# Performance work log

Hardware: AMD Instinct MI355X
Metric: run time of the kernel (lower is better)

Reference implementation:

```python
import jax, jax.numpy as jnp
import numpy as np

N_NODES = 100000
N_EDGES = 3200000
C_IN = 128
C_OUT = 128
K = 4

def setup_inputs() -> dict:
    key = jax.random.key(0)
    k1, k2, k3, k4, k5 = jax.random.split(key, 5)
    x = jax.random.normal(k1, (N_NODES, C_IN), dtype=jnp.float32)
    # per-edge Laplacian values, scaled so the Chebyshev recurrence stays bounded
    lap = jax.random.normal(k2, (N_EDGES,), dtype=jnp.float32) * 0.05
    stdv = 1.0 / np.sqrt(C_IN * K)
    weight = jax.random.uniform(k3, (K, C_IN, C_OUT), dtype=jnp.float32, minval=-stdv, maxval=stdv)
    bias = jax.random.uniform(k4, (C_OUT,), dtype=jnp.float32, minval=-stdv, maxval=stdv)
    edge_index = jax.random.randint(k5, (2, N_EDGES), 0, N_NODES, dtype=jnp.int64)
    return {"x": x, "lap": lap, "weight": weight, "bias": bias,
            "edge_index": edge_index, "num_nodes": N_NODES}

def _spmm(edge_index, lap, num_nodes, x):
    # y[row] += lap_e * x[col] for each edge e = (row, col)
    row, col = edge_index[0], edge_index[1]
    msgs = lap[:, None] * x[col]            # [E, C]
    return jax.ops.segment_sum(msgs, row, num_segments=num_nodes)

def reference(x, lap, weight, bias, edge_index, num_nodes):
    K_ = weight.shape[0]
    Tx_0 = x                                 # T_0(L) x = x
    out = Tx_0 @ weight[0]
    if K_ > 1:
        Tx_1 = _spmm(edge_index, lap, num_nodes, x)   # T_1(L) x = L x
        out = out + Tx_1 @ weight[1]
    for k in range(2, K_):
        Tx_2 = 2.0 * _spmm(edge_index, lap, num_nodes, Tx_1) - Tx_0
        out = out + Tx_2 @ weight[k]
        Tx_0, Tx_1 = Tx_1, Tx_2
    return out + bias
```

## Files before the change

### kernel.cpp

```cpp
#include <hip/hip_runtime.h>

#define N_NODES 100000
#define N_EDGES 3200000
#define ROWS_PAD 100032
#define N_BUCKETS 782
#define BUCKET_SHIFT 7

typedef __attribute__((ext_vector_type(8))) short bf16x8;
typedef __attribute__((ext_vector_type(4))) float f32x4;
typedef __attribute__((ext_vector_type(2))) float f32x2;

__device__ __forceinline__ unsigned short f2bf(float f) {
    unsigned u = __float_as_uint(f);
    unsigned r = (u + 0x7fffu + ((u >> 16) & 1u)) >> 16;
    return (unsigned short)r;
}
__device__ __forceinline__ float bflo(unsigned u) { return __uint_as_float(u << 16); }
__device__ __forceinline__ float bfhi(unsigned u) { return __uint_as_float(u & 0xffff0000u); }

__global__ void __launch_bounds__(256) k_convert_x(const float* __restrict__ x,
                                                   unsigned* __restrict__ xf8) {
    const int QTOT = ROWS_PAD * 32;
    for (int q = blockIdx.x * 256 + threadIdx.x; q < QTOT; q += 1024 * 256) {
        int r = q >> 5;
        f32x4 f = {0.f, 0.f, 0.f, 0.f};
        if (r < N_NODES) f = *(const f32x4*)(x + 4 * (size_t)q);
        int pk = __builtin_amdgcn_cvt_pk_fp8_f32(f.x, f.y, 0, false);
        pk = __builtin_amdgcn_cvt_pk_fp8_f32(f.z, f.w, pk, true);
        xf8[q] = (unsigned)pk;
    }
}

__global__ void k_convert_w(const float* __restrict__ w, unsigned short* __restrict__ wt) {
    int i = blockIdx.x * 256 + threadIdx.x;
    int m = i >> 14, rem = i & 16383, k = rem >> 7, c = rem & 127;
    wt[(m << 14) + (c << 7) + k] = f2bf(w[i]);
}

__global__ void __launch_bounds__(256) k_bhist(const int* __restrict__ ei, int* __restrict__ bcnt) {
    __shared__ int h[N_BUCKETS];
    for (int i = threadIdx.x; i < N_BUCKETS; i += 256) h[i] = 0;
    __syncthreads();
    int base = blockIdx.x * 8192;
#pragma unroll
    for (int i = 0; i < 32; ++i) {
        int e = base + threadIdx.x + i * 256;
        if (e < N_EDGES) atomicAdd(&h[ei[e] >> BUCKET_SHIFT], 1);
    }
    __syncthreads();
    for (int i = threadIdx.x; i < N_BUCKETS; i += 256)
        if (h[i]) atomicAdd(&bcnt[i], h[i]);
}

__global__ void __launch_bounds__(1024) k_bscan(const int* __restrict__ bcnt,
                                                int* __restrict__ bbase,
                                                int* __restrict__ bcursor,
                                                int* __restrict__ rowstart,
                                                int2* __restrict__ ep) {
    __shared__ int s[1024];
    int t = threadIdx.x;
    int v = (t < N_BUCKETS) ? bcnt[t] : 0;
    s[t] = v;
    __syncthreads();
    for (int off = 1; off < 1024; off <<= 1) {
        int tv = (t >= off) ? s[t - off] : 0;
        __syncthreads();
        s[t] += tv;
        __syncthreads();
    }
    if (t < N_BUCKETS) {
        int ex = s[t] - v;
        bbase[t] = ex;
        bcursor[t] = ex;
    }
    if (t == 0) {
        bbase[N_BUCKETS] = N_EDGES;
        rowstart[N_NODES] = N_EDGES;
    }
    if (t < 64) ep[N_EDGES + t] = make_int2(0, 0);
}

__global__ void __launch_bounds__(1024) k_bin(const int* __restrict__ ei,
                                              const float* __restrict__ lap,
                                              int* __restrict__ bcursor,
                                              uint2* __restrict__ ep_tmp) {
    __shared__ int h[N_BUCKETS];
    __shared__ int runbase[N_BUCKETS];
    for (int i = threadIdx.x; i < N_BUCKETS; i += 1024) h[i] = 0;
    __syncthreads();
    int base = blockIdx.x * 16384;
#pragma unroll
    for (int i = 0; i < 16; ++i) {
        int e = base + threadIdx.x + i * 1024;
        if (e < N_EDGES) atomicAdd(&h[ei[e] >> BUCKET_SHIFT], 1);
    }
    __syncthreads();
    for (int i = threadIdx.x; i < N_BUCKETS; i += 1024) {
        int c = h[i];
        runbase[i] = c ? atomicAdd(&bcursor[i], c) : 0;
        h[i] = 0;
    }
    __syncthreads();
#pragma unroll
    for (int i = 0; i < 16; ++i) {
        int e = base + threadIdx.x + i * 1024;
        if (e < N_EDGES) {
            int row = ei[e], col = ei[N_EDGES + e];
            int b = row >> BUCKET_SHIFT;
            int p = runbase[b] + atomicAdd(&h[b], 1);
            ep_tmp[p] = make_uint2(((unsigned)(row & 127) << 17) | (unsigned)col,
                                   __float_as_uint(lap[e]));
        }
    }
}

#define ST_CAP 5120
__global__ void __launch_bounds__(256) k_rsort(const uint2* __restrict__ ep_tmp,
                                               const int* __restrict__ bbase,
                                               int* __restrict__ rowstart,
                                               int2* __restrict__ ep) {
    __shared__ uint2 st[ST_CAP];
    __shared__ int h[128];
    __shared__ int lcur[128];
    int b = blockIdx.x;
    int base = bbase[b], end = bbase[b + 1];
    int n = end - base;
    if (n > ST_CAP) n = ST_CAP;
    for (int i = threadIdx.x; i < n; i += 256) st[i] = ep_tmp[base + i];
    if (threadIdx.x < 128) h[threadIdx.x] = 0;
    __syncthreads();
    for (int i = threadIdx.x; i < n; i += 256) atomicAdd(&h[st[i].x >> 17], 1);
    __syncthreads();
    int t = threadIdx.x;
    int v = (t < 128) ? h[t] : 0;
    for (int off = 1; off < 128; off <<= 1) {
        int tv = (t < 128 && t >= off) ? h[t - off] : 0;
        __syncthreads();
        if (t < 128) h[t] += tv;
        __syncthreads();
    }
    if (t < 128) {
        int ex = h[t] - v;
        int r = (b << BUCKET_SHIFT) + t;
        if (r < N_NODES) rowstart[r] = base + ex;
        lcur[t] = base + ex;
    }
    __syncthreads();
    for (int i = threadIdx.x; i < n; i += 256) {
        uint2 s = st[i];
        int r = s.x >> 17;
        int p = atomicAdd(&lcur[r], 1);
        ep[p] = make_int2((int)(s.x & 0x1FFFFu), (int)s.y);
    }
}

__global__ void __launch_bounds__(256) k_spmm8(
    const unsigned char* __restrict__ xs, const void* __restrict__ z, int zmode,
    unsigned* __restrict__ y8, uint2* __restrict__ yb,
    const int* __restrict__ rowstart, const int2* __restrict__ ep, float a, float b)
{
    int wv = threadIdx.x >> 6, lane = threadIdx.x & 63;
    int r = blockIdx.x * 4 + wv;
    if (r >= N_NODES) return;
    int q = lane >> 4, s = lane & 15;
    unsigned vs8 = (unsigned)s * 8u;
    int bp0 = (q) * 4, bp1 = (4 + q) * 4, bp2 = (8 + q) * 4, bp3 = (12 + q) * 4;
    float acc0 = 0.f, acc1 = 0.f, acc2 = 0.f, acc3 = 0.f;
    float acc4 = 0.f, acc5 = 0.f, acc6 = 0.f, acc7 = 0.f;
    int e0 = rowstart[r], e1 = rowstart[r + 1];
    int cnt = e1 - e0;
    if (cnt > 0) {
        int niter = (cnt + 15) >> 4;
        int nfull = cnt >> 4;
        const char* epb = (const char*)ep;

#define LOADEP(p, itv) do {                                              \
        int _idx = e0 + (itv) * 16 + s;                                  \
        int2 _t = *(const int2*)(epb + (unsigned)_idx * 8u);             \
        if ((itv) >= nfull) {                   \
            bool _v = _idx < e1;                                         \
            _t.x = _v ? _t.x : 0;          \
            _t.y = _v ? _t.y : 0;         \
        }                                                                \
        p = _t;                                                          \
    } while (0)
#define BPERM(cc, ll, p) do {                                            \
        cc[0] = __builtin_amdgcn_ds_bpermute(bp0, (p).x);                \
        cc[1] = __builtin_amdgcn_ds_bpermute(bp1, (p).x);                \
        cc[2] = __builtin_amdgcn_ds_bpermute(bp2, (p).x);                \
        cc[3] = __builtin_amdgcn_ds_bpermute(bp3, (p).x);                \
        ll[0] = __builtin_amdgcn_ds_bpermute(bp0, (p).y);                \
        ll[1] = __builtin_amdgcn_ds_bpermute(bp1, (p).y);                \
        ll[2] = __builtin_amdgcn_ds_bpermute(bp2, (p).y);                \
        ll[3] = __builtin_amdgcn_ds_bpermute(bp3, (p).y);                \
    } while (0)
#define GATHER(G, cc) do {                                               \
        _Pragma("unroll")                                                \
        for (int _u = 0; _u < 4; ++_u)                                   \
            G[_u] = *(const uint2*)(xs + ((((unsigned)cc[_u]) << 7) + vs8)); \
    } while (0)
#define CONSUME(G, ll) do {                                              \
        _Pragma("unroll")                                                \
        for (int _u = 0; _u < 4; ++_u) {                                 \
            float _l = __int_as_float(ll[_u]);                           \
            f32x2 _f0 = __builtin_amdgcn_cvt_pk_f32_fp8((int)G[_u].x, false); \
            f32x2 _f1 = __builtin_amdgcn_cvt_pk_f32_fp8((int)G[_u].x, true);  \
            f32x2 _f2 = __builtin_amdgcn_cvt_pk_f32_fp8((int)G[_u].y, false); \
            f32x2 _f3 = __builtin_amdgcn_cvt_pk_f32_fp8((int)G[_u].y, true);  \
            acc0 += _l * _f0.x; acc1 += _l * _f0.y;                      \
            acc2 += _l * _f1.x; acc3 += _l * _f1.y;                      \
            acc4 += _l * _f2.x; acc5 += _l * _f2.y;                      \
            acc6 += _l * _f3.x; acc7 += _l * _f3.y;                      \
        }                                                                \
    } while (0)

        int2 pA, pB;
        int cA[4], cB[4], lA[4], lB[4];
        uint2 GA[4], GB[4];

        LOADEP(pA, 0);
        BPERM(cA, lA, pA);
        GATHER(GA, cA);
        int it = 0;
        while (it + 2 <= niter) {
            LOADEP(pB, it + 1);
            BPERM(cB, lB, pB);
            GATHER(GB, cB);
            CONSUME(GA, lA);
            if (it + 2 < niter) {
                LOADEP(pA, it + 2);
                BPERM(cA, lA, pA);
                GATHER(GA, cA);
            }
            CONSUME(GB, lB);
            it += 2;
        }
        if (it < niter) CONSUME(GA, lA);
#undef LOADEP
#undef BPERM
#undef GATHER
#undef CONSUME
    }
    acc0 += __shfl(acc0, lane ^ 16, 64); acc1 += __shfl(acc1, lane ^ 16, 64);
    acc2 += __shfl(acc2, lane ^ 16, 64); acc3 += __shfl(acc3, lane ^ 16, 64);
    acc4 += __shfl(acc4, lane ^ 16, 64); acc5 += __shfl(acc5, lane ^ 16, 64);
    acc6 += __shfl(acc6, lane ^ 16, 64); acc7 += __shfl(acc7, lane ^ 16, 64);
    acc0 += __shfl(acc0, lane ^ 32, 64); acc1 += __shfl(acc1, lane ^ 32, 64);
    acc2 += __shfl(acc2, lane ^ 32, 64); acc3 += __shfl(acc3, lane ^ 32, 64);
    acc4 += __shfl(acc4, lane ^ 32, 64); acc5 += __shfl(acc5, lane ^ 32, 64);
    acc6 += __shfl(acc6, lane ^ 32, 64); acc7 += __shfl(acc7, lane ^ 32, 64);
    if (q == 0) {
        float o0 = a * acc0, o1 = a * acc1, o2 = a * acc2, o3 = a * acc3;
        float o4 = a * acc4, o5 = a * acc5, o6 = a * acc6, o7 = a * acc7;
        if (zmode == 1) {
            uint4 zg = *((const uint4*)z + (size_t)r * 16 + s);
            o0 += b * bflo(zg.x); o1 += b * bfhi(zg.x);
            o2 += b * bflo(zg.y); o3 += b * bfhi(zg.y);
            o4 += b * bflo(zg.z); o5 += b * bfhi(zg.z);
            o6 += b * bflo(zg.w); o7 += b * bfhi(zg.w);
        } else if (zmode == 3) {
            const f32x4* zp = (const f32x4*)z + (size_t)r * 32 + s * 2;
            f32x4 z0 = zp[0], z1 = zp[1];
            o0 += b * z0.x; o1 += b * z0.y; o2 += b * z0.z; o3 += b * z0.w;
            o4 += b * z1.x; o5 += b * z1.y; o6 += b * z1.z; o7 += b * z1.w;
        }
        uint4 ob;
        ob.x = (unsigned)f2bf(o0) | ((unsigned)f2bf(o1) << 16);
        ob.y = (unsigned)f2bf(o2) | ((unsigned)f2bf(o3) << 16);
        ob.z = (unsigned)f2bf(o4) | ((unsigned)f2bf(o5) << 16);
        ob.w = (unsigned)f2bf(o6) | ((unsigned)f2bf(o7) << 16);
        *((uint4*)yb + (size_t)r * 16 + s) = ob;
        if (y8) {
            int pk0 = __builtin_amdgcn_cvt_pk_fp8_f32(o0, o1, 0, false);
            pk0 = __builtin_amdgcn_cvt_pk_fp8_f32(o2, o3, pk0, true);
            int pk1 = __builtin_amdgcn_cvt_pk_fp8_f32(o4, o5, 0, false);
            pk1 = __builtin_amdgcn_cvt_pk_fp8_f32(o6, o7, pk1, true);
            *((uint2*)y8 + (size_t)r * 16 + s) = make_uint2((unsigned)pk0, (unsigned)pk1);
        }
    }
}

__global__ void __launch_bounds__(256, 4) k_gemm4(
    const float* __restrict__ x,
    const unsigned short* __restrict__ t1,
    const unsigned short* __restrict__ t2,
    const unsigned short* __restrict__ t3,
    const unsigned short* __restrict__ wt,
    float* __restrict__ out, const float* __restrict__ bias)
{
    __shared__ float cbuf[4][16 * 132];
    int wv = threadIdx.x >> 6, lane = threadIdx.x & 63;
    int m = lane & 15, quad = lane >> 4;
    int r0 = blockIdx.x * 64 + wv * 16;
    int row = r0 + m;
    int rowc = (row >= N_NODES) ? (N_NODES - 1) : row;

    f32x4 acc[8];
#pragma unroll
    for (int ct = 0; ct < 8; ++ct) acc[ct] = (f32x4){0.f, 0.f, 0.f, 0.f};

    {
        bf16x8 a[4];
        {
            const float* p = x + (size_t)rowc * 128 + quad * 8;
#pragma unroll
            for (int kk = 0; kk < 4; ++kk) {
                f32x4 u = *(const f32x4*)(p + kk * 32);
                f32x4 v = *(const f32x4*)(p + kk * 32 + 4);
                bf16x8 fr;
                fr[0] = (short)f2bf(u.x); fr[1] = (short)f2bf(u.y);
                fr[2] = (short)f2bf(u.z); fr[3] = (short)f2bf(u.w);
                fr[4] = (short)f2bf(v.x); fr[5] = (short)f2bf(v.y);
                fr[6] = (short)f2bf(v.z); fr[7] = (short)f2bf(v.w);
                a[kk] = fr;
            }
        }
#pragma unroll
        for (int ct = 0; ct < 8; ++ct) {
            const short* B = (const short*)wt + (ct * 16 + m) * 128 + quad * 8;
#pragma unroll
            for (int kk = 0; kk < 4; ++kk)
                acc[ct] = __builtin_amdgcn_mfma_f32_16x16x32_bf16(
                    a[kk], *(const bf16x8*)(B + kk * 32), acc[ct], 0, 0, 0);
        }
    }
    const unsigned short* tA[3] = {t1, t2, t3};
#pragma unroll
    for (int t = 0; t < 3; ++t) {
        bf16x8 a[4];
        {
            const short* p = (const short*)tA[t] + (size_t)row * 128 + quad * 8;
#pragma unroll
            for (int kk = 0; kk < 4; ++kk) a[kk] = *(const bf16x8*)(p + kk * 32);
        }
        const short* Wb = (const short*)wt + (t + 1) * 16384;
#pragma unroll
        for (int ct = 0; ct < 8; ++ct) {
            const short* B = Wb + (ct * 16 + m) * 128 + quad * 8;
#pragma unroll
            for (int kk = 0; kk < 4; ++kk)
                acc[ct] = __builtin_amdgcn_mfma_f32_16x16x32_bf16(
                    a[kk], *(const bf16x8*)(B + kk * 32), acc[ct], 0, 0, 0);
        }
    }
    float* cw = &cbuf[wv][0];
#pragma unroll
    for (int ct = 0; ct < 8; ++ct)
#pragma unroll
        for (int i = 0; i < 4; ++i)
            cw[(quad * 4 + i) * 132 + ct * 16 + m] = acc[ct][i];
    int er = lane >> 2, ec = (lane & 3) * 32;
    int gr = r0 + er;
#pragma unroll
    for (int j = 0; j < 8; ++j) {
        f32x4 v = *(f32x4*)(cw + er * 132 + ec + j * 4);
        f32x4 bb = *(const f32x4*)(bias + ec + j * 4);
        v.x += bb.x; v.y += bb.y; v.z += bb.z; v.w += bb.w;
        if (gr < N_NODES)
            *(f32x4*)(out + (size_t)gr * 128 + ec + j * 4) = v;
    }
}

extern "C" void kernel_launch(void* const* d_in, const int* in_sizes, int n_in,
                              void* d_out, int out_size, void* d_ws, size_t ws_size,
                              hipStream_t stream) {
    const float* x    = (const float*)d_in[0];
    const float* lap  = (const float*)d_in[1];
    const float* w    = (const float*)d_in[2];
    const float* bias = (const float*)d_in[3];
    const int*   ei   = (const int*)d_in[4];
    float* out = (float*)d_out;

    char* ws = (char*)d_ws;
    const size_t SZ_BF = (size_t)ROWS_PAD * 128 * 2;
    const size_t SZ_F8 = (size_t)ROWS_PAD * 128;
    const size_t SZ_EP = SZ_BF + 1024;
    int2* ep            = (int2*)(ws);
    unsigned char* xf8  = (unsigned char*)(ws + SZ_EP);
    unsigned char* t1_8 = (unsigned char*)(ws + SZ_EP + SZ_F8);
    unsigned char* t3_b = (unsigned char*)(ws + SZ_EP);
    unsigned char* t1_b = (unsigned char*)(ws + SZ_EP + SZ_BF);
    unsigned char* t2_8 = (unsigned char*)(ws + SZ_EP + 2 * SZ_BF);
    unsigned char* t2_b = (unsigned char*)(ws + SZ_EP + 2 * SZ_BF + SZ_F8);
    uint2* ep_tmp       = (uint2*)(ws + SZ_EP + 2 * SZ_BF);
    char* p = ws + SZ_EP + 3 * SZ_BF + SZ_F8;
    int* rowstart = (int*)p; p += 400128;
    int* bcnt     = (int*)p; p += 3200;
    int* bbase    = (int*)p; p += 3200;
    int* bcursor  = (int*)p; p += 3200;
    unsigned short* wt = (unsigned short*)p;

    hipMemsetAsync(bcnt, 0, N_BUCKETS * sizeof(int), stream);
    k_convert_x<<<1024, 256, 0, stream>>>(x, (unsigned*)xf8);
    k_convert_w<<<256, 256, 0, stream>>>(w, wt);
    k_bhist<<<(N_EDGES + 8191) / 8192, 256, 0, stream>>>(ei, bcnt);
    k_bscan<<<1, 1024, 0, stream>>>(bcnt, bbase, bcursor, rowstart, ep);
    k_bin<<<(N_EDGES + 16383) / 16384, 1024, 0, stream>>>(ei, lap, bcursor, ep_tmp);
    k_rsort<<<N_BUCKETS, 256, 0, stream>>>(ep_tmp, bbase, rowstart, ep);

    k_spmm8<<<ROWS_PAD / 4, 256, 0, stream>>>(xf8, nullptr, 0,
        (unsigned*)t1_8, (uint2*)t1_b, rowstart, ep, 1.f, 0.f);
    k_spmm8<<<ROWS_PAD / 4, 256, 0, stream>>>(t1_8, x, 3,
        (unsigned*)t2_8, (uint2*)t2_b, rowstart, ep, 2.f, -1.f);
    k_spmm8<<<ROWS_PAD / 4, 256, 0, stream>>>(t2_8, t1_b, 1,
        nullptr, (uint2*)t3_b, rowstart, ep, 2.f, -1.f);
    k_gemm4<<<ROWS_PAD / 64, 256, 0, stream>>>(x, (const unsigned short*)t1_b,
        (const unsigned short*)t2_b, (const unsigned short*)t3_b, wt, out, bias);
}
```

Before: 575.0 us.

## Stage weights in swizzled LDS and preload all A fragments in gemm4

The final GEMM kernel now copies the weight matrices into shared memory in two 64KB phases using an XOR swizzle. MFMA B operands are read from LDS instead of straight from global memory. All four A-fragment sets (x converted to bf16, t1, t2, t3) are loaded up front so their global latency overlaps. Launch bounds drop to 2 blocks per SM to make room for the extra registers and the 64KB of LDS, at the cost of lower occupancy and added barriers.

```diff
diff --git a/kernel.cpp b/kernel.cpp
--- a/kernel.cpp
+++ b/kernel.cpp
@@ -280,7 +280,7 @@
     }
 }
 
-__global__ void __launch_bounds__(256, 4) k_gemm4(
+__global__ void __launch_bounds__(256, 2) k_gemm4(
     const float* __restrict__ x,
     const unsigned short* __restrict__ t1,
     const unsigned short* __restrict__ t2,
@@ -288,62 +288,78 @@
     const unsigned short* __restrict__ wt,
     float* __restrict__ out, const float* __restrict__ bias)
 {
-    __shared__ float cbuf[4][16 * 132];
+    __shared__ uint4 ldsq[4096];
+    char* lds = (char*)ldsq;
     int wv = threadIdx.x >> 6, lane = threadIdx.x & 63;
     int m = lane & 15, quad = lane >> 4;
     int r0 = blockIdx.x * 64 + wv * 16;
     int row = r0 + m;
     int rowc = (row >= N_NODES) ? (N_NODES - 1) : row;
 
+    bf16x8 a0[4], a1[4], a2[4], a3[4];
+    {
+        const float* p = x + (size_t)rowc * 128 + quad * 8;
+#pragma unroll
+        for (int kk = 0; kk < 4; ++kk) {
+            f32x4 u = *(const f32x4*)(p + kk * 32);
+            f32x4 v = *(const f32x4*)(p + kk * 32 + 4);
+            bf16x8 fr;
+            fr[0] = (short)f2bf(u.x); fr[1] = (short)f2bf(u.y);
+            fr[2] = (short)f2bf(u.z); fr[3] = (short)f2bf(u.w);
+            fr[4] = (short)f2bf(v.x); fr[5] = (short)f2bf(v.y);
+            fr[6] = (short)f2bf(v.z); fr[7] = (short)f2bf(v.w);
+            a0[kk] = fr;
+        }
+    }
+    {
+        const short* p = (const short*)t1 + (size_t)row * 128 + quad * 8;
+#pragma unroll
+        for (int kk = 0; kk < 4; ++kk) a1[kk] = *(const bf16x8*)(p + kk * 32);
+    }
+    {
+        const short* p = (const short*)t2 + (size_t)row * 128 + quad * 8;
+#pragma unroll
+        for (int kk = 0; kk < 4; ++kk) a2[kk] = *(const bf16x8*)(p + kk * 32);
+    }
+    {
+        const short* p = (const short*)t3 + (size_t)row * 128 + quad * 8;
+#pragma unroll
+        for (int kk = 0; kk < 4; ++kk) a3[kk] = *(const bf16x8*)(p + kk * 32);
+    }
+
     f32x4 acc[8];
 #pragma unroll
     for (int ct = 0; ct < 8; ++ct) acc[ct] = (f32x4){0.f, 0.f, 0.f, 0.f};
 
-    {
-        bf16x8 a[4];
-        {
-            const float* p = x + (size_t)rowc * 128 + quad * 8;
-#pragma unroll
-            for (int kk = 0; kk < 4; ++kk) {
-                f32x4 u = *(const f32x4*)(p + kk * 32);
-                f32x4 v = *(const f32x4*)(p + kk * 32 + 4);
-                bf16x8 fr;
-                fr[0] = (short)f2bf(u.x); fr[1] = (short)f2bf(u.y);
-                fr[2] = (short)f2bf(u.z); fr[3] = (short)f2bf(u.w);
-                fr[4] = (short)f2bf(v.x); fr[5] = (short)f2bf(v.y);
-                fr[6] = (short)f2bf(v.z); fr[7] = (short)f2bf(v.w);
-                a[kk] = fr;
+#pragma unroll
+    for (int ph = 0; ph < 2; ++ph) {
+        if (ph) __syncthreads();
+        const char* src = (const char*)wt + ph * 65536;
+#pragma unroll
+        for (int i = 0; i < 16; ++i) {
+            int idx = i * 256 + (int)threadIdx.x;
+            int g = idx >> 4, j = idx & 15;
+            *(uint4*)(lds + g * 256 + ((unsigned)(j ^ (g & 15)) << 4)) =
+                *(const uint4*)(src + idx * 16);
+        }
+        __syncthreads();
+#pragma unroll
+        for (int tl = 0; tl < 2; ++tl) {
+#pragma unroll
+            for (int ct = 0; ct < 8; ++ct) {
+#pragma unroll
+                for (int kk = 0; kk < 4; ++kk) {
+                    const bf16x8* B = (const bf16x8*)(lds + tl * 32768 + ct * 4096
+                        + m * 256 + ((unsigned)(((quad + kk * 4) ^ m)) << 4));
+                    bf16x8 av = (ph == 0) ? (tl == 0 ? a0[kk] : a1[kk])
+                                          : (tl == 0 ? a2[kk] : a3[kk]);
+                    acc[ct] = __builtin_amdgcn_mfma_f32_16x16x32_bf16(av, *B, acc[ct], 0, 0, 0);
+                }
             }
         }
-#pragma unroll
-        for (int ct = 0; ct < 8; ++ct) {
-            const short* B = (const short*)wt + (ct * 16 + m) * 128 + quad * 8;
-#pragma unroll
-            for (int kk = 0; kk < 4; ++kk)
-                acc[ct] = __builtin_amdgcn_mfma_f32_16x16x32_bf16(
-                    a[kk], *(const bf16x8*)(B + kk * 32), acc[ct], 0, 0, 0);
-        }
-    }
-    const unsigned short* tA[3] = {t1, t2, t3};
-#pragma unroll
-    for (int t = 0; t < 3; ++t) {
-        bf16x8 a[4];
-        {
-            const short* p = (const short*)tA[t] + (size_t)row * 128 + quad * 8;
-#pragma unroll
-            for (int kk = 0; kk < 4; ++kk) a[kk] = *(const bf16x8*)(p + kk * 32);
-        }
-        const short* Wb = (const short*)wt + (t + 1) * 16384;
-#pragma unroll
-        for (int ct = 0; ct < 8; ++ct) {
-            const short* B = Wb + (ct * 16 + m) * 128 + quad * 8;
-#pragma unroll
-            for (int kk = 0; kk < 4; ++kk)
-                acc[ct] = __builtin_amdgcn_mfma_f32_16x16x32_bf16(
-                    a[kk], *(const bf16x8*)(B + kk * 32), acc[ct], 0, 0, 0);
-        }
-    }
-    float* cw = &cbuf[wv][0];
+    }
+    __syncthreads();
+    float* cw = (float*)lds + wv * (16 * 132);
 #pragma unroll
     for (int ct = 0; ct < 8; ++ct)
 #pragma unroll
```

Result: faster. 502.0 us (-12.7%).
